# Kernel tuning notes

Measured on AMD Instinct MI355X. Metric: run time of the kernel, lower is better.

Reference implementation:

```python
import jax, jax.numpy as jnp
import numpy as np

N_QUBITS = 10
N_LAYERS = 4
DIM = 2 ** N_QUBITS  # 1024
IN_FEATURES = 512
OUT_FEATURES = 64
BATCH = 4096


def setup_inputs() -> dict:
    key = jax.random.key(0)
    ks = jax.random.split(key, 6)
    return {
        "x": jax.random.normal(ks[0], (BATCH, IN_FEATURES), dtype=jnp.float32),
        "W_pre": jax.random.normal(ks[1], (DIM, IN_FEATURES), dtype=jnp.float32) / np.float32(np.sqrt(IN_FEATURES)),
        "b_pre": jnp.zeros((DIM,), dtype=jnp.float32),
        "q_weights": jax.random.normal(ks[2], (N_LAYERS, N_QUBITS, 3), dtype=jnp.float32),
        "W_post": jax.random.normal(ks[3], (OUT_FEATURES, N_QUBITS), dtype=jnp.float32) / np.float32(np.sqrt(N_QUBITS)),
        "b_post": jnp.zeros((OUT_FEATURES,), dtype=jnp.float32),
    }


def _rot_matrices(w):
    # w: [L, n, 3] -> PennyLane Rot(phi, theta, omega) = RZ(omega) RY(theta) RZ(phi)
    phi, theta, omega = w[..., 0], w[..., 1], w[..., 2]
    c = jnp.cos(theta / 2).astype(jnp.complex64)
    s = jnp.sin(theta / 2).astype(jnp.complex64)
    e_mm = jnp.exp(-0.5j * (phi + omega))
    e_pp = jnp.exp(0.5j * (phi + omega))
    e_pm = jnp.exp(0.5j * (phi - omega))
    e_mp = jnp.exp(-0.5j * (phi - omega))
    row0 = jnp.stack([e_mm * c, -e_pm * s], axis=-1)
    row1 = jnp.stack([e_mp * s, e_pp * c], axis=-1)
    return jnp.stack([row0, row1], axis=-2)  # [L, n, 2, 2] complex64


def _apply_1q(psi, U, wire):
    # psi: [B, 2, 2, ..., 2]; apply 2x2 unitary U on qubit `wire` (axis wire+1)
    axis = wire + 1
    psi = jnp.moveaxis(psi, axis, -1)
    psi = psi @ U.T  # new[a] = sum_b U[a,b] psi[b]
    return jnp.moveaxis(psi, -1, axis)


def _cnot(psi, control, target):
    ca, ta = control + 1, target + 1
    p0 = jax.lax.index_in_dim(psi, 0, ca, keepdims=True)
    p1 = jax.lax.index_in_dim(psi, 1, ca, keepdims=True)
    p1 = jnp.flip(p1, axis=ta)  # flip target amplitudes where control = 1
    return jnp.concatenate([p0, p1], axis=ca)


def _quantum_forward(amps, q_weights):
    # AmplitudeEmbedding(normalize=True) + StronglyEntanglingLayers + PauliZ expvals, batched.
    B = amps.shape[0]
    norm = jnp.sqrt(jnp.sum(amps * amps, axis=1, keepdims=True))
    psi = (amps / norm).astype(jnp.complex64).reshape((B,) + (2,) * N_QUBITS)
    U = _rot_matrices(q_weights)
    for l in range(N_LAYERS):
        for w in range(N_QUBITS):
            psi = _apply_1q(psi, U[l, w], w)
        r = (l % (N_QUBITS - 1)) + 1  # PennyLane default ranges
        for w in range(N_QUBITS):
            psi = _cnot(psi, w, (w + r) % N_QUBITS)
    probs = psi.real ** 2 + psi.imag ** 2
    axes_all = tuple(range(1, N_QUBITS + 1))
    z = []
    for i in range(N_QUBITS):
        other = tuple(a for a in axes_all if a != i + 1)
        marg = jnp.sum(probs, axis=other)  # [B, 2]
        z.append(marg[:, 0] - marg[:, 1])
    return jnp.stack(z, axis=1)  # [B, n_qubits]


def reference(x, W_pre, b_pre, q_weights, W_post, b_post):
    h = jax.nn.relu(x @ W_pre.T + b_pre)          # [B, 2^n]
    z = _quantum_forward(h, q_weights)            # [B, n_qubits]
    return z @ W_post.T + b_post                  # [B, out_features]
```

## Files before the change

### kernel.cpp

```cpp
#include <hip/hip_runtime.h>
#include <hip/hip_bf16.h>
#include <math.h>

#define NQ   10
#define DIM  1024
#define NL   4
#define INF  512
#define OUTF 64
#define MBATCH 4096

typedef _Float16 half8 __attribute__((ext_vector_type(8)));
typedef float f32x4 __attribute__((ext_vector_type(4)));
typedef float f32x2 __attribute__((ext_vector_type(2)));

#define WS_H16  0
#define WS_X16  (8u * 1024u * 1024u)
#define WS_W16  (12u * 1024u * 1024u)
#define WS_ROT  (13u * 1024u * 1024u)
#define WS_TAB  (13u * 1024u * 1024u + 4096u)

#define HD __host__ __device__

HD constexpr int fstep(int j, int r) {
    for (int w2 = NQ - 1; w2 >= 0; --w2) {
        const int cb = 9 - w2;
        const int tb = 9 - ((w2 + r) % NQ);
        j ^= ((j >> cb) & 1) << tb;
    }
    return j;
}
HD constexpr int ifstep(int j, int r) {
    for (int w2 = 0; w2 < NQ; ++w2) {
        const int cb = 9 - w2;
        const int tb = 9 - ((w2 + r) % NQ);
        j ^= ((j >> cb) & 1) << tb;
    }
    return j;
}
HD constexpr int sigma_fwd(int l, int x) {
    for (int t = l - 1; t >= 0; --t) x = fstep(x, t + 1);
    return x;
}
HD constexpr int sigma_inv(int l, int s) {
    for (int t = 0; t < l; ++t) s = ifstep(s, t + 1);
    return s;
}
constexpr int gate_m(int l, int b) { return sigma_fwd(l, 1 << b); }
constexpr int gate_g(int l, int b) {
    int g = 0;
    for (int j = 0; j < NQ; ++j)
        if ((sigma_inv(l, 1 << j) >> b) & 1) g |= 1 << j;
    return g;
}
struct QM { int v[NQ]; };
constexpr QM make_qm() {
    QM q{};
    for (int w = 0; w < NQ; ++w) {
        const int B = 9 - w;
        int m = 0;
        for (int j = 0; j < NQ; ++j)
            if ((sigma_inv(NL, 1 << j) >> B) & 1) m |= 1 << j;
        q.v[w] = m;
    }
    return q;
}
constexpr QM QMASKS = make_qm();

constexpr int mask_at(int t) { return gate_m(t / 10, 9 - (t % 10)); }
constexpr int pick_wbit() {
    int best = 9, bc = 1000;
    for (int j = 3; j <= 9; ++j) {
        int c = 0;
        for (int t = 0; t < 40; ++t) c += (mask_at(t) >> j) & 1;
        if (c < bc) { bc = c; best = j; }
    }
    return best;
}
constexpr int WBIT = pick_wbit();
struct LP { int v[6]; };
constexpr LP make_lpos() {
    LP p{}; int n = 0;
    for (int j = 3; j <= 9; ++j) if (j != WBIT) p.v[n++] = j;
    return p;
}
constexpr LP LPOS = make_lpos();
constexpr int lx_extract(int m) {
    int r = 0;
    for (int t = 0; t < 6; ++t) if ((m >> LPOS.v[t]) & 1) r |= 1 << t;
    return r;
}

__global__ __launch_bounds__(256) void setup_kernel(
    const float* __restrict__ x, const float* __restrict__ w,
    const float* __restrict__ qw, _Float16* __restrict__ x16,
    _Float16* __restrict__ w16, float2* __restrict__ rot,
    float2* __restrict__ tabs)
{
    const int bid = blockIdx.x;
    const int tid = threadIdx.x;
    if (bid < 1024) {
        const int base = bid * 2048 + tid * 8;
        float4 a = *reinterpret_cast<const float4*>(x + base);
        float4 b = *reinterpret_cast<const float4*>(x + base + 4);
        half8 o = {(_Float16)a.x, (_Float16)a.y, (_Float16)a.z, (_Float16)a.w,
                   (_Float16)b.x, (_Float16)b.y, (_Float16)b.z, (_Float16)b.w};
        *reinterpret_cast<half8*>(x16 + base) = o;
    } else if (bid < 1280) {
        const int base = (bid - 1024) * 2048 + tid * 8;
        float4 a = *reinterpret_cast<const float4*>(w + base);
        float4 b = *reinterpret_cast<const float4*>(w + base + 4);
        half8 o = {(_Float16)a.x, (_Float16)a.y, (_Float16)a.z, (_Float16)a.w,
                   (_Float16)b.x, (_Float16)b.y, (_Float16)b.z, (_Float16)b.w};
        *reinterpret_cast<half8*>(w16 + base) = o;
    } else {
        if (tid < NL * NQ) {
            float s, c; sincosf(0.5f * qw[tid * 3 + 1], &s, &c);
            rot[tid] = float2{c, s};
        }
        for (int u = 0; u < 4; ++u) {
            const int s_ = (tid << 2) + u;
            float a = 0.f;
            for (int w2 = 0; w2 < NQ; ++w2)
                a += qw[w2 * 3 + 0] * (((s_ >> (9 - w2)) & 1) ? 1.f : -1.f);
            float si, co; sincosf(0.5f * a, &si, &co);
            tabs[s_] = float2{co, si};
            for (int l = 0; l < 3; ++l) {
                const int j  = sigma_inv(l, s_);
                const int ip = sigma_inv(l + 1, s_);
                float b = 0.f;
                for (int w2 = 0; w2 < NQ; ++w2) {
                    b += qw[(l * NQ + w2) * 3 + 2]       * (((j  >> (9 - w2)) & 1) ? 1.f : -1.f);
                    b += qw[((l + 1) * NQ + w2) * 3 + 0] * (((ip >> (9 - w2)) & 1) ? 1.f : -1.f);
                }
                sincosf(0.5f * b, &si, &co);
                tabs[(l + 1) * DIM + s_] = float2{co, si};
            }
        }
    }
}

__global__ __launch_bounds__(256) void gemm16_kernel(
    const _Float16* __restrict__ X, const _Float16* __restrict__ W,
    const float* __restrict__ bias, _Float16* __restrict__ H)
{
    constexpr int BM = 128, BN = 64, BK = 32, LDP = BK + 8;
    __shared__ _Float16 As[BM][LDP];
    __shared__ _Float16 Bs[BN][LDP];

    const int tid = threadIdx.x;
    const int wave = tid >> 6, lane = tid & 63;
    const int wm = wave >> 1, wn = wave & 1;
    const int l15 = lane & 15, lk = (lane >> 4) * 8;

    const int arow = tid >> 1, ahalf = tid & 1;
    const int brow = tid & 63, bseg = tid >> 6;

    const _Float16* ag = X + (size_t)(blockIdx.x * BM + arow) * INF + ahalf * 16;
    const _Float16* bg = W + (size_t)(blockIdx.y * BN + brow) * INF + bseg * 8;

    f32x4 acc[4][2] = {};

    for (int k0 = 0; k0 < INF; k0 += BK) {
        half8 av0 = *reinterpret_cast<const half8*>(ag + k0);
        half8 av1 = *reinterpret_cast<const half8*>(ag + k0 + 8);
        half8 bv  = *reinterpret_cast<const half8*>(bg + k0);
        __syncthreads();
        *reinterpret_cast<half8*>(&As[arow][ahalf * 16])     = av0;
        *reinterpret_cast<half8*>(&As[arow][ahalf * 16 + 8]) = av1;
        *reinterpret_cast<half8*>(&Bs[brow][bseg * 8])       = bv;
        __syncthreads();
        half8 bfr0 = *reinterpret_cast<const half8*>(&Bs[wn * 32 + l15][lk]);
        half8 bfr1 = *reinterpret_cast<const half8*>(&Bs[wn * 32 + 16 + l15][lk]);
#pragma unroll
        for (int mi = 0; mi < 4; ++mi) {
            half8 afr = *reinterpret_cast<const half8*>(&As[wm * 64 + mi * 16 + l15][lk]);
            acc[mi][0] = __builtin_amdgcn_mfma_f32_16x16x32_f16(afr, bfr0, acc[mi][0], 0, 0, 0);
            acc[mi][1] = __builtin_amdgcn_mfma_f32_16x16x32_f16(afr, bfr1, acc[mi][1], 0, 0, 0);
        }
    }

    const int crow0 = blockIdx.x * BM + wm * 64;
    const int ccol0 = blockIdx.y * BN + wn * 32;
#pragma unroll
    for (int ni = 0; ni < 2; ++ni) {
        const int col = ccol0 + ni * 16 + l15;
        const float bb = bias[col];
#pragma unroll
        for (int mi = 0; mi < 4; ++mi) {
#pragma unroll
            for (int r = 0; r < 4; ++r) {
                const int row = crow0 + mi * 16 + (lane >> 4) * 4 + r;
                const float o = fmaxf(acc[mi][ni][r] + bb, 0.f);
                H[(size_t)row * DIM + col] = (_Float16)o;
            }
        }
    }
}

template<int MHI>
__device__ __forceinline__ int lxi(int v, int lane) {
    if constexpr (MHI == 0)
        return v;
    else if constexpr (MHI == 1)
        return __builtin_amdgcn_mov_dpp(v, 0xB1, 0xF, 0xF, false);
    else if constexpr (MHI == 2)
        return __builtin_amdgcn_mov_dpp(v, 0x4E, 0xF, 0xF, false);
    else if constexpr (MHI == 3)
        return __builtin_amdgcn_mov_dpp(v, 0x1B, 0xF, 0xF, false);
    else if constexpr (MHI == 8)
        return __builtin_amdgcn_mov_dpp(v, 0x128, 0xF, 0xF, false);
    else if constexpr (MHI < 32)
        return __builtin_amdgcn_ds_swizzle(v, 0x1F | (MHI << 10));
    else
        return __builtin_amdgcn_ds_bpermute((lane ^ MHI) << 2, v);
}

template<int MHI>
__device__ __forceinline__ float lxf(float v, int lane) {
    return __int_as_float(lxi<MHI>(__float_as_int(v), lane));
}

__device__ __forceinline__ float allred(float v, int lane) {
    v += lxf<1>(v, lane);
    v += lxf<2>(v, lane);
    v += lxf<4>(v, lane);
    v += lxf<8>(v, lane);
    v += lxf<16>(v, lane);
    v += lxf<32>(v, lane);
    return v;
}

template<int L, int W>
__device__ __forceinline__ void apply_ry(f32x2 rr[4], f32x2 ii[4],
                                         const float2* __restrict__ rot,
                                         int lane, int wave,
                                         f32x4 (*buf)[2][64])
{
    constexpr int b = 9 - W;
    constexpr int m = gate_m(L, b);
    constexpr int g = gate_g(L, b);
    constexpr int MW    = (m >> WBIT) & 1;
    constexpr int MLANE = lx_extract(m);
    constexpr int MREG  = m & 7;
    constexpr int GW    = (g >> WBIT) & 1;
    constexpr int GLANE = lx_extract(g);
    constexpr int GREG  = g & 7;

    const float2 cs = rot[L * NQ + W];
    int hli = __builtin_popcount(lane & GLANE) & 1;
    if constexpr (GW) hli ^= wave;
    const float sp = hli ? cs.y : -cs.y;
    const float sn = -sp;
    const f32x2 C = {cs.x, cs.x};

    float pr[8], pi[8];
    if constexpr (MW == 0) {
#pragma unroll
        for (int k = 0; k < 8; ++k) {
            const int kp = k ^ MREG;
            const float vr = (kp & 1) ? rr[kp >> 1].y : rr[kp >> 1].x;
            const float vi = (kp & 1) ? ii[kp >> 1].y : ii[kp >> 1].x;
            pr[k] = lxf<MLANE>(vr, lane);
            pi[k] = lxf<MLANE>(vi, lane);
        }
    } else {
        buf[0][wave][lane] = f32x4{rr[0].x, rr[0].y, rr[1].x, rr[1].y};
        buf[1][wave][lane] = f32x4{rr[2].x, rr[2].y, rr[3].x, rr[3].y};
        buf[2][wave][lane] = f32x4{ii[0].x, ii[0].y, ii[1].x, ii[1].y};
        buf[3][wave][lane] = f32x4{ii[2].x, ii[2].y, ii[3].x, ii[3].y};
        __syncthreads();
        const int pl = lane ^ MLANE;
        const int pw = wave ^ 1;
        const f32x4 R0 = buf[0][pw][pl];
        const f32x4 R1 = buf[1][pw][pl];
        const f32x4 I0 = buf[2][pw][pl];
        const f32x4 I1 = buf[3][pw][pl];
        __syncthreads();
#pragma unroll
        for (int k = 0; k < 8; ++k) {
            const int kp = k ^ MREG;
            pr[k] = (kp & 4) ? R1[kp & 3] : R0[kp & 3];
            pi[k] = (kp & 4) ? I1[kp & 3] : I0[kp & 3];
        }
    }
#pragma unroll
    for (int j = 0; j < 4; ++j) {
        const int k0 = 2 * j, k1 = 2 * j + 1;
        const float s0 = (__builtin_popcount(k0 & GREG) & 1) ? sn : sp;
        const float s1 = (__builtin_popcount(k1 & GREG) & 1) ? sn : sp;
        const f32x2 S = {s0, s1};
        const f32x2 PR = {pr[k0], pr[k1]};
        const f32x2 PI = {pi[k0], pi[k1]};
        rr[j] = C * rr[j] + S * PR;
        ii[j] = C * ii[j] + S * PI;
    }
}

__device__ __forceinline__ void apply_diag_reg(f32x2 rr[4], f32x2 ii[4],
                                               const f32x4 d[4])
{
#pragma unroll
    for (int j = 0; j < 4; ++j) {
        const f32x2 CR = {d[j].x, d[j].z};
        const f32x2 CI = {d[j].y, d[j].w};
        const f32x2 R = rr[j], I = ii[j];
        rr[j] = R * CR - I * CI;
        ii[j] = I * CR + R * CI;
    }
}

template<int L>
__device__ __forceinline__ void apply_layer(f32x2 rr[4], f32x2 ii[4],
                                            const float2* __restrict__ rot,
                                            int lane, int wave,
                                            f32x4 (*buf)[2][64])
{
    apply_ry<L, 0>(rr, ii, rot, lane, wave, buf);
    apply_ry<L, 1>(rr, ii, rot, lane, wave, buf);
    apply_ry<L, 2>(rr, ii, rot, lane, wave, buf);
    apply_ry<L, 3>(rr, ii, rot, lane, wave, buf);
    apply_ry<L, 4>(rr, ii, rot, lane, wave, buf);
    apply_ry<L, 5>(rr, ii, rot, lane, wave, buf);
    apply_ry<L, 6>(rr, ii, rot, lane, wave, buf);
    apply_ry<L, 7>(rr, ii, rot, lane, wave, buf);
    apply_ry<L, 8>(rr, ii, rot, lane, wave, buf);
    apply_ry<L, 9>(rr, ii, rot, lane, wave, buf);
}

__global__ __launch_bounds__(128, 8) void quantum_kernel(
    const _Float16* __restrict__ Hbuf, const float2* __restrict__ rot,
    const float2* __restrict__ tabs, const float* __restrict__ W_post,
    const float* __restrict__ b_post, float* __restrict__ out)
{
    __shared__ f32x4 buf[4][2][64];
    __shared__ float sred[34];

    const int lane = threadIdx.x;
    const int wave = threadIdx.y;
    const int row  = blockIdx.x;

    int pb = wave << WBIT;
#pragma unroll
    for (int t = 0; t < 6; ++t) pb |= ((lane >> t) & 1) << LPOS.v[t];

    const f32x4* t0 = reinterpret_cast<const f32x4*>(tabs + pb);
    const f32x4* t1 = reinterpret_cast<const f32x4*>(tabs + 1 * DIM + pb);
    const f32x4* t2 = reinterpret_cast<const f32x4*>(tabs + 2 * DIM + pb);
    const f32x4* t3 = reinterpret_cast<const f32x4*>(tabs + 3 * DIM + pb);

    const _Float16* hr = Hbuf + (size_t)row * DIM + pb;
    f32x2 A[4];
    f32x4 d[4];
    {
        half8 h0 = *reinterpret_cast<const half8*>(hr);
#pragma unroll
        for (int j = 0; j < 4; ++j) {
            A[j] = f32x2{(float)h0[2 * j], (float)h0[2 * j + 1]};
            d[j] = t0[j];
        }
    }

    f32x2 n2 = f32x2{0.f, 0.f};
#pragma unroll
    for (int j = 0; j < 4; ++j) n2 += A[j] * A[j];
    float nw = allred(n2.x + n2.y, lane);
    if (lane == 0) sred[32 + wave] = nw;
    __syncthreads();
    const float inv_nrm = 1.0f / (sred[32] + sred[33]);

    f32x2 rr[4], ii[4];
#pragma unroll
    for (int j = 0; j < 4; ++j) {
        rr[j] = A[j] * f32x2{d[j].x, d[j].z};
        ii[j] = A[j] * f32x2{d[j].y, d[j].w};
    }

#pragma unroll
    for (int j = 0; j < 4; ++j) d[j] = t1[j];
    apply_layer<0>(rr, ii, rot, lane, wave, buf);
    apply_diag_reg(rr, ii, d);
#pragma unroll
    for (int j = 0; j < 4; ++j) d[j] = t2[j];
    apply_layer<1>(rr, ii, rot, lane, wave, buf);
    apply_diag_reg(rr, ii, d);
#pragma unroll
    for (int j = 0; j < 4; ++j) d[j] = t3[j];
    apply_layer<2>(rr, ii, rot, lane, wave, buf);
    apply_diag_reg(rr, ii, d);
    apply_layer<3>(rr, ii, rot, lane, wave, buf);

    f32x2 P[4];
#pragma unroll
    for (int j = 0; j < 4; ++j) P[j] = rr[j] * rr[j] + ii[j] * ii[j];

    float z[NQ];
#pragma unroll
    for (int w = 0; w < NQ; ++w) {
        const int q = QMASKS.v[w];
        const int qw_ = (q >> WBIT) & 1;
        const int qlane = lx_extract(q);
        const int qreg = q & 7;
        float zl = 0.f;
#pragma unroll
        for (int j = 0; j < 4; ++j) {
            const float s0 = (__builtin_popcount((2 * j) & qreg) & 1) ? -1.f : 1.f;
            const float s1 = (__builtin_popcount((2 * j + 1) & qreg) & 1) ? -1.f : 1.f;
            zl += s0 * P[j].x + s1 * P[j].y;
        }
        int neg = __builtin_popcount(lane & qlane) & 1;
        neg ^= (wave & qw_);
        if (neg) zl = -zl;
        z[w] = allred(zl, lane);
    }
    if (lane == 0) {
#pragma unroll
        for (int w = 0; w < NQ; ++w) sred[wave * 16 + w] = z[w];
    }
    __syncthreads();

    if (wave == 0) {
        float o = b_post[lane];
#pragma unroll
        for (int w = 0; w < NQ; ++w)
            o = fmaf((sred[w] + sred[16 + w]) * inv_nrm, W_post[lane * NQ + w], o);
        out[(size_t)row * OUTF + lane] = o;
    }
}

extern "C" void kernel_launch(void* const* d_in, const int* in_sizes, int n_in,
                              void* d_out, int out_size, void* d_ws, size_t ws_size,
                              hipStream_t stream) {
    const float* x      = (const float*)d_in[0];
    const float* W_pre  = (const float*)d_in[1];
    const float* b_pre  = (const float*)d_in[2];
    const float* qw     = (const float*)d_in[3];
    const float* W_post = (const float*)d_in[4];
    const float* b_post = (const float*)d_in[5];
    float* out = (float*)d_out;

    char* ws = (char*)d_ws;
    _Float16* h16 = (_Float16*)(ws + WS_H16);
    _Float16* x16 = (_Float16*)(ws + WS_X16);
    _Float16* w16 = (_Float16*)(ws + WS_W16);
    float2*   rot = (float2*)  (ws + WS_ROT);
    float2*   tabs= (float2*)  (ws + WS_TAB);

    setup_kernel<<<1281, 256, 0, stream>>>(x, W_pre, qw, x16, w16, rot, tabs);
    dim3 g1(MBATCH / 128, DIM / 64);
    gemm16_kernel<<<g1, 256, 0, stream>>>(x16, w16, b_pre, h16);
    quantum_kernel<<<MBATCH, dim3(64, 2), 0, stream>>>(h16, rot, tabs, W_post, b_post, out);
}
```

Measured before the change: 65.05 us.

## Map each batch row to a single wavefront with 16 amplitudes per lane

The quantum statevector kernel now simulates one batch row per 64-lane wave, holding 16 complex amplitudes per lane instead of 8 amplitudes split across two waves. Gates are handled with register permutations and cross-lane exchanges only, which removes the shared-memory staging and __syncthreads used when a gate crossed the wave bit. Blocks now carry four independent rows. The cost is roughly double the register use per lane, which may lower occupancy.

```diff
diff --git a/kernel.cpp b/kernel.cpp
--- a/kernel.cpp
+++ b/kernel.cpp
@@ -65,30 +65,6 @@
     return q;
 }
 constexpr QM QMASKS = make_qm();
-
-constexpr int mask_at(int t) { return gate_m(t / 10, 9 - (t % 10)); }
-constexpr int pick_wbit() {
-    int best = 9, bc = 1000;
-    for (int j = 3; j <= 9; ++j) {
-        int c = 0;
-        for (int t = 0; t < 40; ++t) c += (mask_at(t) >> j) & 1;
-        if (c < bc) { bc = c; best = j; }
-    }
-    return best;
-}
-constexpr int WBIT = pick_wbit();
-struct LP { int v[6]; };
-constexpr LP make_lpos() {
-    LP p{}; int n = 0;
-    for (int j = 3; j <= 9; ++j) if (j != WBIT) p.v[n++] = j;
-    return p;
-}
-constexpr LP LPOS = make_lpos();
-constexpr int lx_extract(int m) {
-    int r = 0;
-    for (int t = 0; t < 6; ++t) if ((m >> LPOS.v[t]) & 1) r |= 1 << t;
-    return r;
-}
 
 __global__ __launch_bounds__(256) void setup_kernel(
     const float* __restrict__ x, const float* __restrict__ w,
@@ -231,63 +207,36 @@
 }
 
 template<int L, int W>
-__device__ __forceinline__ void apply_ry(f32x2 rr[4], f32x2 ii[4],
+__device__ __forceinline__ void apply_ry(f32x2 rr[8], f32x2 ii[8],
                                          const float2* __restrict__ rot,
-                                         int lane, int wave,
-                                         f32x4 (*buf)[2][64])
+                                         int lane)
 {
     constexpr int b = 9 - W;
     constexpr int m = gate_m(L, b);
     constexpr int g = gate_g(L, b);
-    constexpr int MW    = (m >> WBIT) & 1;
-    constexpr int MLANE = lx_extract(m);
-    constexpr int MREG  = m & 7;
-    constexpr int GW    = (g >> WBIT) & 1;
-    constexpr int GLANE = lx_extract(g);
-    constexpr int GREG  = g & 7;
+    constexpr int MHI = m >> 4, MLO = m & 15;
+    constexpr int GHI = g >> 4, GLO = g & 15;
 
     const float2 cs = rot[L * NQ + W];
-    int hli = __builtin_popcount(lane & GLANE) & 1;
-    if constexpr (GW) hli ^= wave;
-    const float sp = hli ? cs.y : -cs.y;
+    const bool hl = (__builtin_popcount(lane & GHI) & 1) != 0;
+    const float sp = hl ? cs.y : -cs.y;
     const float sn = -sp;
     const f32x2 C = {cs.x, cs.x};
 
-    float pr[8], pi[8];
-    if constexpr (MW == 0) {
-#pragma unroll
-        for (int k = 0; k < 8; ++k) {
-            const int kp = k ^ MREG;
-            const float vr = (kp & 1) ? rr[kp >> 1].y : rr[kp >> 1].x;
-            const float vi = (kp & 1) ? ii[kp >> 1].y : ii[kp >> 1].x;
-            pr[k] = lxf<MLANE>(vr, lane);
-            pi[k] = lxf<MLANE>(vi, lane);
-        }
-    } else {
-        buf[0][wave][lane] = f32x4{rr[0].x, rr[0].y, rr[1].x, rr[1].y};
-        buf[1][wave][lane] = f32x4{rr[2].x, rr[2].y, rr[3].x, rr[3].y};
-        buf[2][wave][lane] = f32x4{ii[0].x, ii[0].y, ii[1].x, ii[1].y};
-        buf[3][wave][lane] = f32x4{ii[2].x, ii[2].y, ii[3].x, ii[3].y};
-        __syncthreads();
-        const int pl = lane ^ MLANE;
-        const int pw = wave ^ 1;
-        const f32x4 R0 = buf[0][pw][pl];
-        const f32x4 R1 = buf[1][pw][pl];
-        const f32x4 I0 = buf[2][pw][pl];
-        const f32x4 I1 = buf[3][pw][pl];
-        __syncthreads();
-#pragma unroll
-        for (int k = 0; k < 8; ++k) {
-            const int kp = k ^ MREG;
-            pr[k] = (kp & 4) ? R1[kp & 3] : R0[kp & 3];
-            pi[k] = (kp & 4) ? I1[kp & 3] : I0[kp & 3];
-        }
-    }
-#pragma unroll
-    for (int j = 0; j < 4; ++j) {
+    float pr[16], pi[16];
+#pragma unroll
+    for (int k = 0; k < 16; ++k) {
+        const int kp = k ^ MLO;
+        const float vr = (kp & 1) ? rr[kp >> 1].y : rr[kp >> 1].x;
+        const float vi = (kp & 1) ? ii[kp >> 1].y : ii[kp >> 1].x;
+        pr[k] = lxf<MHI>(vr, lane);
+        pi[k] = lxf<MHI>(vi, lane);
+    }
+#pragma unroll
+    for (int j = 0; j < 8; ++j) {
         const int k0 = 2 * j, k1 = 2 * j + 1;
-        const float s0 = (__builtin_popcount(k0 & GREG) & 1) ? sn : sp;
-        const float s1 = (__builtin_popcount(k1 & GREG) & 1) ? sn : sp;
+        const float s0 = (__builtin_popcount(k0 & GLO) & 1) ? sn : sp;
+        const float s1 = (__builtin_popcount(k1 & GLO) & 1) ? sn : sp;
         const f32x2 S = {s0, s1};
         const f32x2 PR = {pr[k0], pr[k1]};
         const f32x2 PI = {pi[k0], pi[k1]};
@@ -296,11 +245,11 @@
     }
 }
 
-__device__ __forceinline__ void apply_diag_reg(f32x2 rr[4], f32x2 ii[4],
-                                               const f32x4 d[4])
-{
-#pragma unroll
-    for (int j = 0; j < 4; ++j) {
+__device__ __forceinline__ void apply_diag_reg(f32x2 rr[8], f32x2 ii[8],
+                                               const f32x4 d[8])
+{
+#pragma unroll
+    for (int j = 0; j < 8; ++j) {
         const f32x2 CR = {d[j].x, d[j].z};
         const f32x2 CI = {d[j].y, d[j].w};
         const f32x2 R = rr[j], I = ii[j];
@@ -310,121 +259,102 @@
 }
 
 template<int L>
-__device__ __forceinline__ void apply_layer(f32x2 rr[4], f32x2 ii[4],
+__device__ __forceinline__ void apply_layer(f32x2 rr[8], f32x2 ii[8],
                                             const float2* __restrict__ rot,
-                                            int lane, int wave,
-                                            f32x4 (*buf)[2][64])
-{
-    apply_ry<L, 0>(rr, ii, rot, lane, wave, buf);
-    apply_ry<L, 1>(rr, ii, rot, lane, wave, buf);
-    apply_ry<L, 2>(rr, ii, rot, lane, wave, buf);
-    apply_ry<L, 3>(rr, ii, rot, lane, wave, buf);
-    apply_ry<L, 4>(rr, ii, rot, lane, wave, buf);
-    apply_ry<L, 5>(rr, ii, rot, lane, wave, buf);
-    apply_ry<L, 6>(rr, ii, rot, lane, wave, buf);
-    apply_ry<L, 7>(rr, ii, rot, lane, wave, buf);
-    apply_ry<L, 8>(rr, ii, rot, lane, wave, buf);
-    apply_ry<L, 9>(rr, ii, rot, lane, wave, buf);
-}
-
-__global__ __launch_bounds__(128, 8) void quantum_kernel(
+                                            int lane)
+{
+    apply_ry<L, 0>(rr, ii, rot, lane);
+    apply_ry<L, 1>(rr, ii, rot, lane);
+    apply_ry<L, 2>(rr, ii, rot, lane);
+    apply_ry<L, 3>(rr, ii, rot, lane);
+    apply_ry<L, 4>(rr, ii, rot, lane);
+    apply_ry<L, 5>(rr, ii, rot, lane);
+    apply_ry<L, 6>(rr, ii, rot, lane);
+    apply_ry<L, 7>(rr, ii, rot, lane);
+    apply_ry<L, 8>(rr, ii, rot, lane);
+    apply_ry<L, 9>(rr, ii, rot, lane);
+}
+
+__global__ __launch_bounds__(256) void quantum_kernel(
     const _Float16* __restrict__ Hbuf, const float2* __restrict__ rot,
     const float2* __restrict__ tabs, const float* __restrict__ W_post,
     const float* __restrict__ b_post, float* __restrict__ out)
 {
-    __shared__ f32x4 buf[4][2][64];
-    __shared__ float sred[34];
-
     const int lane = threadIdx.x;
-    const int wave = threadIdx.y;
-    const int row  = blockIdx.x;
-
-    int pb = wave << WBIT;
-#pragma unroll
-    for (int t = 0; t < 6; ++t) pb |= ((lane >> t) & 1) << LPOS.v[t];
-
+    const int row  = blockIdx.x * 4 + threadIdx.y;
+
+    const int pb = lane << 4;
     const f32x4* t0 = reinterpret_cast<const f32x4*>(tabs + pb);
     const f32x4* t1 = reinterpret_cast<const f32x4*>(tabs + 1 * DIM + pb);
     const f32x4* t2 = reinterpret_cast<const f32x4*>(tabs + 2 * DIM + pb);
     const f32x4* t3 = reinterpret_cast<const f32x4*>(tabs + 3 * DIM + pb);
 
     const _Float16* hr = Hbuf + (size_t)row * DIM + pb;
-    f32x2 A[4];
-    f32x4 d[4];
+    f32x2 A[8];
+    f32x4 d[8];
     {
         half8 h0 = *reinterpret_cast<const half8*>(hr);
+        half8 h1 = *reinterpret_cast<const half8*>(hr + 8);
 #pragma unroll
         for (int j = 0; j < 4; ++j) {
-            A[j] = f32x2{(float)h0[2 * j], (float)h0[2 * j + 1]};
-            d[j] = t0[j];
-        }
+            A[j]     = f32x2{(float)h0[2 * j], (float)h0[2 * j + 1]};
+            A[j + 4] = f32x2{(float)h1[2 * j], (float)h1[2 * j + 1]};
+        }
+#pragma unroll
+        for (int j = 0; j < 8; ++j) d[j] = t0[j];
     }
 
     f32x2 n2 = f32x2{0.f, 0.f};
 #pragma unroll
-    for (int j = 0; j < 4; ++j) n2 += A[j] * A[j];
-    float nw = allred(n2.x + n2.y, lane);
-    if (lane == 0) sred[32 + wave] = nw;
-    __syncthreads();
-    const float inv_nrm = 1.0f / (sred[32] + sred[33]);
-
-    f32x2 rr[4], ii[4];
-#pragma unroll
-    for (int j = 0; j < 4; ++j) {
+    for (int j = 0; j < 8; ++j) n2 += A[j] * A[j];
+    const float inv_nrm = 1.0f / allred(n2.x + n2.y, lane);
+
+    f32x2 rr[8], ii[8];
+#pragma unroll
+    for (int j = 0; j < 8; ++j) {
         rr[j] = A[j] * f32x2{d[j].x, d[j].z};
         ii[j] = A[j] * f32x2{d[j].y, d[j].w};
     }
 
 #pragma unroll
-    for (int j = 0; j < 4; ++j) d[j] = t1[j];
-    apply_layer<0>(rr, ii, rot, lane, wave, buf);
+    for (int j = 0; j < 8; ++j) d[j] = t1[j];
+    apply_layer<0>(rr, ii, rot, lane);
     apply_diag_reg(rr, ii, d);
 #pragma unroll
-    for (int j = 0; j < 4; ++j) d[j] = t2[j];
-    apply_layer<1>(rr, ii, rot, lane, wave, buf);
+    for (int j = 0; j < 8; ++j) d[j] = t2[j];
+    apply_layer<1>(rr, ii, rot, lane);
     apply_diag_reg(rr, ii, d);
 #pragma unroll
-    for (int j = 0; j < 4; ++j) d[j] = t3[j];
-    apply_layer<2>(rr, ii, rot, lane, wave, buf);
+    for (int j = 0; j < 8; ++j) d[j] = t3[j];
+    apply_layer<2>(rr, ii, rot, lane);
     apply_diag_reg(rr, ii, d);
-    apply_layer<3>(rr, ii, rot, lane, wave, buf);
-
-    f32x2 P[4];
-#pragma unroll
-    for (int j = 0; j < 4; ++j) P[j] = rr[j] * rr[j] + ii[j] * ii[j];
+    apply_layer<3>(rr, ii, rot, lane);
+
+    f32x2 P[8];
+#pragma unroll
+    for (int j = 0; j < 8; ++j) P[j] = rr[j] * rr[j] + ii[j] * ii[j];
 
     float z[NQ];
 #pragma unroll
     for (int w = 0; w < NQ; ++w) {
         const int q = QMASKS.v[w];
-        const int qw_ = (q >> WBIT) & 1;
-        const int qlane = lx_extract(q);
-        const int qreg = q & 7;
+        const int qhi = q >> 4, qlo = q & 15;
         float zl = 0.f;
 #pragma unroll
-        for (int j = 0; j < 4; ++j) {
-            const float s0 = (__builtin_popcount((2 * j) & qreg) & 1) ? -1.f : 1.f;
-            const float s1 = (__builtin_popcount((2 * j + 1) & qreg) & 1) ? -1.f : 1.f;
+        for (int j = 0; j < 8; ++j) {
+            const float s0 = (__builtin_popcount((2 * j) & qlo) & 1) ? -1.f : 1.f;
+            const float s1 = (__builtin_popcount((2 * j + 1) & qlo) & 1) ? -1.f : 1.f;
             zl += s0 * P[j].x + s1 * P[j].y;
         }
-        int neg = __builtin_popcount(lane & qlane) & 1;
-        neg ^= (wave & qw_);
-        if (neg) zl = -zl;
-        z[w] = allred(zl, lane);
-    }
-    if (lane == 0) {
-#pragma unroll
-        for (int w = 0; w < NQ; ++w) sred[wave * 16 + w] = z[w];
-    }
-    __syncthreads();
-
-    if (wave == 0) {
-        float o = b_post[lane];
-#pragma unroll
-        for (int w = 0; w < NQ; ++w)
-            o = fmaf((sred[w] + sred[16 + w]) * inv_nrm, W_post[lane * NQ + w], o);
-        out[(size_t)row * OUTF + lane] = o;
-    }
+        if (__builtin_popcount(lane & qhi) & 1) zl = -zl;
+        z[w] = allred(zl, lane) * inv_nrm;
+    }
+
+    float o = b_post[lane];
+#pragma unroll
+    for (int w = 0; w < NQ; ++w)
+        o = fmaf(z[w], W_post[lane * NQ + w], o);
+    out[(size_t)row * OUTF + lane] = o;
 }
 
 extern "C" void kernel_launch(void* const* d_in, const int* in_sizes, int n_in,
@@ -448,5 +378,5 @@
     setup_kernel<<<1281, 256, 0, stream>>>(x, W_pre, qw, x16, w16, rot, tabs);
     dim3 g1(MBATCH / 128, DIM / 64);
     gemm16_kernel<<<g1, 256, 0, stream>>>(x16, w16, b_pre, h16);
-    quantum_kernel<<<MBATCH, dim3(64, 2), 0, stream>>>(h16, rot, tabs, W_post, b_post, out);
-}
+    quantum_kernel<<<MBATCH / 4, dim3(64, 4), 0, stream>>>(h16, rot, tabs, W_post, b_post, out);
+}
```

Result: faster. 63.49 us (-2.4%).
